# Kernel tuning notes

Hardware: AMD Instinct MI355X
Metric: run time of the kernel (lower is better)

Reference implementation:

```python
import jax, jax.numpy as jnp
import numpy as np

RATE_NUM = 8
MAX_RATE = 256
C = 256


def setup_inputs() -> dict:
    key = jax.random.key(0)
    k1, k2, k3, k4 = jax.random.split(key, 4)
    B, H, W = 4, 32, 32
    x = jax.random.normal(k1, (B, MAX_RATE, H, W), dtype=jnp.float32)
    indexes = jax.random.randint(k2, (B * H * W,), 0, RATE_NUM, dtype=jnp.int64)
    # kaiming_normal_(a=sqrt(5)) on (rate_num, max_rate, C): fan_in = C (last dim),
    # gain = sqrt(2/(1+a^2)) = sqrt(1/3), std = gain/sqrt(fan_in)
    std = np.sqrt(1.0 / 3.0) / np.sqrt(C)
    weight = jax.random.normal(k3, (RATE_NUM, MAX_RATE, C), dtype=jnp.float32) * std
    bound = 1.0 / np.sqrt(RATE_NUM)
    bias = jax.random.uniform(k4, (RATE_NUM, C), dtype=jnp.float32, minval=-bound, maxval=bound)
    return {"x": x, "indexes": indexes, "weight": weight, "bias": bias}


def reference(x, indexes, weight, bias):
    B, R, H, W = x.shape  # R == max_rate
    L = H * W
    x_blr = x.reshape(B, R, L).transpose(0, 2, 1)          # (B, L, R)
    w = weight[indexes].reshape(B, L, R, -1)               # (B, L, R, C)
    b = bias[indexes].reshape(B, L, -1)                    # (B, L, C)
    out = jnp.einsum('blr,blrc->blc', x_blr, w) + b        # per-token GEMV
    return out.reshape(B, H, W, -1).transpose(0, 3, 1, 2)  # (B, C, H, W)
```

## Files before the change

### kernel.cpp

```cpp
#include <hip/hip_runtime.h>


#define C_DIM 256
#define KD    256
#define CB    128
#define LB    128
#define LDP   132

typedef __attribute__((ext_vector_type(8))) short bf16x8;
typedef __attribute__((ext_vector_type(4))) float f32x4;

__device__ inline unsigned pk2(float a, float b) {
    union { float f; unsigned u; } x, y; x.f = a; y.f = b;
    return ((x.u + 0x8000u) >> 16) | ((y.u + 0x8000u) & 0xFFFF0000u);
}

__global__ __launch_bounds__(256) void fused_mfma_kernel(
    const float* __restrict__ x,
    const int*   __restrict__ idx,
    const float* __restrict__ weight,
    const float* __restrict__ bias,
    float*       __restrict__ out)
{
    const int t    = threadIdx.x;
    const int lane = t & 63;
    const int wav  = t >> 6;
    const int quad = lane >> 4;
    const int li   = lane & 15;

    const int j    = blockIdx.z;
    const int cb0  = blockIdx.x * CB;
    const int lg0b = blockIdx.y * LB;
    const int b    = lg0b >> 10;
    const int l0b  = lg0b & 1023;

    __shared__ unsigned Asl[32 * LDP];
    __shared__ unsigned Bsl[32 * LDP];

    const int c_locb = (wav & 1) * 64;
    const int l_locb = (wav >> 1) * 64;

    const float* __restrict__ wbase = weight + j * (KD * C_DIM) + cb0;
    const float* __restrict__ xbase = x + (b << 18) + l0b;

    const int sc4  = (t & 31) * 4;
    const int srow = t >> 5;

    f32x4 acc[4][4];
    #pragma unroll
    for (int mt = 0; mt < 4; ++mt)
        #pragma unroll
        for (int nt = 0; nt < 4; ++nt)
            acc[mt][nt] = (f32x4){0.f, 0.f, 0.f, 0.f};

    for (int p = 0; p < 4; ++p) {
        const int k0 = p * 64;

        #pragma unroll
        for (int i = 0; i < 4; ++i) {
            const int kp = i * 8 + srow;
            const int k  = k0 + kp * 2;
            const float4 a0 = *(const float4*)(wbase + k * C_DIM + sc4);
            const float4 a1 = *(const float4*)(wbase + (k + 1) * C_DIM + sc4);
            const float4 b0 = *(const float4*)(xbase + (k << 10) + sc4);
            const float4 b1 = *(const float4*)(xbase + ((k + 1) << 10) + sc4);
            uint4 pa, pb;
            pa.x = pk2(a0.x, a1.x); pa.y = pk2(a0.y, a1.y);
            pa.z = pk2(a0.z, a1.z); pa.w = pk2(a0.w, a1.w);
            pb.x = pk2(b0.x, b1.x); pb.y = pk2(b0.y, b1.y);
            pb.z = pk2(b0.z, b1.z); pb.w = pk2(b0.w, b1.w);
            *(uint4*)&Asl[kp * LDP + sc4] = pa;
            *(uint4*)&Bsl[kp * LDP + sc4] = pb;
        }
        __syncthreads();

        #pragma unroll
        for (int h = 0; h < 2; ++h) {
            const int rbase = h * 16 + quad * 4;
            bf16x8 af[4], bfr[4];
            #pragma unroll
            for (int mt = 0; mt < 4; ++mt) {
                const int cl = c_locb + mt * 16 + li;
                uint4 u;
                u.x = Asl[(rbase + 0) * LDP + cl];
                u.y = Asl[(rbase + 1) * LDP + cl];
                u.z = Asl[(rbase + 2) * LDP + cl];
                u.w = Asl[(rbase + 3) * LDP + cl];
                af[mt] = __builtin_bit_cast(bf16x8, u);
            }
            #pragma unroll
            for (int nt = 0; nt < 4; ++nt) {
                const int ll = l_locb + nt * 16 + li;
                uint4 u;
                u.x = Bsl[(rbase + 0) * LDP + ll];
                u.y = Bsl[(rbase + 1) * LDP + ll];
                u.z = Bsl[(rbase + 2) * LDP + ll];
                u.w = Bsl[(rbase + 3) * LDP + ll];
                bfr[nt] = __builtin_bit_cast(bf16x8, u);
            }
            #pragma unroll
            for (int mt = 0; mt < 4; ++mt)
                #pragma unroll
                for (int nt = 0; nt < 4; ++nt)
                    acc[mt][nt] = __builtin_amdgcn_mfma_f32_16x16x32_bf16(
                        af[mt], bfr[nt], acc[mt][nt], 0, 0, 0);
        }
        __syncthreads();
    }

    bool keep[4];
    int  lgv[4];
    #pragma unroll
    for (int nt = 0; nt < 4; ++nt) {
        lgv[nt]  = lg0b + l_locb + nt * 16 + li;
        keep[nt] = (idx[lgv[nt]] == j);
    }
    #pragma unroll
    for (int mt = 0; mt < 4; ++mt) {
        const int cb = cb0 + c_locb + mt * 16 + quad * 4;
        const float4 bb = *(const float4*)(bias + j * C_DIM + cb);
        #pragma unroll
        for (int nt = 0; nt < 4; ++nt) {
            if (!keep[nt]) continue;
            float* __restrict__ op = out + (b << 18) + (cb << 10) + (lgv[nt] & 1023);
            op[0 << 10] = acc[mt][nt][0] + bb.x;
            op[1 << 10] = acc[mt][nt][1] + bb.y;
            op[2 << 10] = acc[mt][nt][2] + bb.z;
            op[3 << 10] = acc[mt][nt][3] + bb.w;
        }
    }
}

extern "C" void kernel_launch(void* const* d_in, const int* in_sizes, int n_in,
                              void* d_out, int out_size, void* d_ws, size_t ws_size,
                              hipStream_t stream)
{
    const float* x      = (const float*)d_in[0];
    const int*   idx    = (const int*)  d_in[1];
    const float* weight = (const float*)d_in[2];
    const float* bias   = (const float*)d_in[3];
    float*       out    = (float*)      d_out;

    fused_mfma_kernel<<<dim3(2, 32, 8), 256, 0, stream>>>(x, idx, weight, bias, out);
}
```

Before: 74.08 us.

## Double-buffer LDS tiles and prefetch next K slice into registers

Adds a two-stage pipeline to the K loop. The next 64-deep slice of weight and x is loaded into registers while MFMAs run on the current LDS buffer, then packed into the alternate LDS buffer. One of the two barriers per iteration is removed. Launch bounds now request two blocks per CU, which limits registers while the prefetch arrays raise register pressure, so spills are possible.

```diff
diff --git a/kernel.cpp b/kernel.cpp
--- a/kernel.cpp
+++ b/kernel.cpp
@@ -15,7 +15,7 @@
     return ((x.u + 0x8000u) >> 16) | ((y.u + 0x8000u) & 0xFFFF0000u);
 }
 
-__global__ __launch_bounds__(256) void fused_mfma_kernel(
+__global__ __launch_bounds__(256, 2) void fused_mfma_kernel(
     const float* __restrict__ x,
     const int*   __restrict__ idx,
     const float* __restrict__ weight,
@@ -34,8 +34,8 @@
     const int b    = lg0b >> 10;
     const int l0b  = lg0b & 1023;
 
-    __shared__ unsigned Asl[32 * LDP];
-    __shared__ unsigned Bsl[32 * LDP];
+    __shared__ unsigned Asl[2][32 * LDP];
+    __shared__ unsigned Bsl[2][32 * LDP];
 
     const int c_locb = (wav & 1) * 64;
     const int l_locb = (wav >> 1) * 64;
@@ -53,27 +53,46 @@
         for (int nt = 0; nt < 4; ++nt)
             acc[mt][nt] = (f32x4){0.f, 0.f, 0.f, 0.f};
 
+    float4 a0[4], a1[4], b0[4], b1[4];
+    #pragma unroll
+    for (int i = 0; i < 4; ++i) {
+        const int kp = i * 8 + srow;
+        const int k  = kp * 2;
+        a0[i] = *(const float4*)(wbase + k * C_DIM + sc4);
+        a1[i] = *(const float4*)(wbase + (k + 1) * C_DIM + sc4);
+        b0[i] = *(const float4*)(xbase + (k << 10) + sc4);
+        b1[i] = *(const float4*)(xbase + ((k + 1) << 10) + sc4);
+    }
+    #pragma unroll
+    for (int i = 0; i < 4; ++i) {
+        const int kp = i * 8 + srow;
+        uint4 pa, pb;
+        pa.x = pk2(a0[i].x, a1[i].x); pa.y = pk2(a0[i].y, a1[i].y);
+        pa.z = pk2(a0[i].z, a1[i].z); pa.w = pk2(a0[i].w, a1[i].w);
+        pb.x = pk2(b0[i].x, b1[i].x); pb.y = pk2(b0[i].y, b1[i].y);
+        pb.z = pk2(b0[i].z, b1[i].z); pb.w = pk2(b0[i].w, b1[i].w);
+        *(uint4*)&Asl[0][kp * LDP + sc4] = pa;
+        *(uint4*)&Bsl[0][kp * LDP + sc4] = pb;
+    }
+    __syncthreads();
+
+    #pragma unroll
     for (int p = 0; p < 4; ++p) {
-        const int k0 = p * 64;
+        if (p < 3) {
+            const int k0 = (p + 1) * 64;
+            #pragma unroll
+            for (int i = 0; i < 4; ++i) {
+                const int kp = i * 8 + srow;
+                const int k  = k0 + kp * 2;
+                a0[i] = *(const float4*)(wbase + k * C_DIM + sc4);
+                a1[i] = *(const float4*)(wbase + (k + 1) * C_DIM + sc4);
+                b0[i] = *(const float4*)(xbase + (k << 10) + sc4);
+                b1[i] = *(const float4*)(xbase + ((k + 1) << 10) + sc4);
+            }
+        }
 
-        #pragma unroll
-        for (int i = 0; i < 4; ++i) {
-            const int kp = i * 8 + srow;
-            const int k  = k0 + kp * 2;
-            const float4 a0 = *(const float4*)(wbase + k * C_DIM + sc4);
-            const float4 a1 = *(const float4*)(wbase + (k + 1) * C_DIM + sc4);
-            const float4 b0 = *(const float4*)(xbase + (k << 10) + sc4);
-            const float4 b1 = *(const float4*)(xbase + ((k + 1) << 10) + sc4);
-            uint4 pa, pb;
-            pa.x = pk2(a0.x, a1.x); pa.y = pk2(a0.y, a1.y);
-            pa.z = pk2(a0.z, a1.z); pa.w = pk2(a0.w, a1.w);
-            pb.x = pk2(b0.x, b1.x); pb.y = pk2(b0.y, b1.y);
-            pb.z = pk2(b0.z, b1.z); pb.w = pk2(b0.w, b1.w);
-            *(uint4*)&Asl[kp * LDP + sc4] = pa;
-            *(uint4*)&Bsl[kp * LDP + sc4] = pb;
-        }
-        __syncthreads();
-
+        const unsigned* __restrict__ Ab = Asl[p & 1];
+        const unsigned* __restrict__ Bb = Bsl[p & 1];
         #pragma unroll
         for (int h = 0; h < 2; ++h) {
             const int rbase = h * 16 + quad * 4;
@@ -82,20 +101,20 @@
             for (int mt = 0; mt < 4; ++mt) {
                 const int cl = c_locb + mt * 16 + li;
                 uint4 u;
-                u.x = Asl[(rbase + 0) * LDP + cl];
-                u.y = Asl[(rbase + 1) * LDP + cl];
-                u.z = Asl[(rbase + 2) * LDP + cl];
-                u.w = Asl[(rbase + 3) * LDP + cl];
+                u.x = Ab[(rbase + 0) * LDP + cl];
+                u.y = Ab[(rbase + 1) * LDP + cl];
+                u.z = Ab[(rbase + 2) * LDP + cl];
+                u.w = Ab[(rbase + 3) * LDP + cl];
                 af[mt] = __builtin_bit_cast(bf16x8, u);
             }
             #pragma unroll
             for (int nt = 0; nt < 4; ++nt) {
                 const int ll = l_locb + nt * 16 + li;
                 uint4 u;
-                u.x = Bsl[(rbase + 0) * LDP + ll];
-                u.y = Bsl[(rbase + 1) * LDP + ll];
-                u.z = Bsl[(rbase + 2) * LDP + ll];
-                u.w = Bsl[(rbase + 3) * LDP + ll];
+                u.x = Bb[(rbase + 0) * LDP + ll];
+                u.y = Bb[(rbase + 1) * LDP + ll];
+                u.z = Bb[(rbase + 2) * LDP + ll];
+                u.w = Bb[(rbase + 3) * LDP + ll];
                 bfr[nt] = __builtin_bit_cast(bf16x8, u);
             }
             #pragma unroll
@@ -105,7 +124,22 @@
                     acc[mt][nt] = __builtin_amdgcn_mfma_f32_16x16x32_bf16(
                         af[mt], bfr[nt], acc[mt][nt], 0, 0, 0);
         }
-        __syncthreads();
+
+        if (p < 3) {
+            const int q = (p + 1) & 1;
+            #pragma unroll
+            for (int i = 0; i < 4; ++i) {
+                const int kp = i * 8 + srow;
+                uint4 pa, pb;
+                pa.x = pk2(a0[i].x, a1[i].x); pa.y = pk2(a0[i].y, a1[i].y);
+                pa.z = pk2(a0[i].z, a1[i].z); pa.w = pk2(a0[i].w, a1[i].w);
+                pb.x = pk2(b0[i].x, b1[i].x); pb.y = pk2(b0[i].y, b1[i].y);
+                pb.z = pk2(b0[i].z, b1[i].z); pb.w = pk2(b0[i].w, b1[i].w);
+                *(uint4*)&Asl[q][kp * LDP + sc4] = pa;
+                *(uint4*)&Bsl[q][kp * LDP + sc4] = pb;
+            }
+            __syncthreads();
+        }
     }
 
     bool keep[4];
```

Result: faster. 72.37 us (-2.3%).
